# Kernel optimization log

Measured on AMD Instinct MI355X. Metric: run time of the kernel, lower is better.

## Reference

```python
import jax, jax.numpy as jnp
import numpy as np

DEPTH = 16
HID = 256
INP = 256
K = 2  # arity of the complete binary tree
TOTAL = (1 << (DEPTH + 1)) - 1  # 131071 nodes, level-order indexed


def setup_inputs() -> dict:
    key = jax.random.key(0)
    ks = jax.random.split(key, 14)
    s = 1.0 / np.sqrt(HID)
    inp = {
        "x": jax.random.normal(ks[0], (TOTAL, INP), jnp.float32),
        "Wi": jax.random.normal(ks[1], (HID, INP), jnp.float32) * s,
        "bi": jax.random.normal(ks[2], (HID,), jnp.float32) * s,
        "Wf": jax.random.normal(ks[3], (HID, INP), jnp.float32) * s,
        "bf": jax.random.normal(ks[4], (HID,), jnp.float32) * s,
        "Wo": jax.random.normal(ks[5], (HID, INP), jnp.float32) * s,
        "bo": jax.random.normal(ks[6], (HID,), jnp.float32) * s,
        "Wu": jax.random.normal(ks[7], (HID, INP), jnp.float32) * s,
        "bu": jax.random.normal(ks[8], (HID,), jnp.float32) * s,
        "Ui": jax.random.normal(ks[9], (HID, HID), jnp.float32) * s,
        "Uo": jax.random.normal(ks[10], (HID, HID), jnp.float32) * s,
        "Uu": jax.random.normal(ks[11], (HID, HID), jnp.float32) * s,
        "Wfk": jax.random.normal(ks[12], (K, HID, HID), jnp.float32) * s,
        "depth": DEPTH,
    }
    return inp


def reference(x, Wi, bi, Wf, bf, Wo, bo, Wu, bu, Ui, Uo, Uu, Wfk, depth):
    sig = jax.nn.sigmoid
    H = Ui.shape[0]
    # leaf level: leaf_forward (no recurrent terms)
    start, n = (1 << depth) - 1, 1 << depth
    xs = x[start:start + n]                      # [n, INP]
    i = sig(xs @ Wi.T + bi)
    o = sig(xs @ Wo.T + bo)
    u = jnp.tanh(xs @ Wu.T + bu)
    c = i * u
    h = o * jnp.tanh(c)
    # internal levels, bottom-up
    for d in range(depth - 1, -1, -1):
        start, n = (1 << d) - 1, 1 << d
        xs = x[start:start + n]                  # [n, INP]
        hc = h.reshape(n, K, H)                  # children h (level-order)
        cc = c.reshape(n, K, H)                  # children c
        Hs = hc.sum(axis=1)                      # sum over children, [n, H]
        i = sig(xs @ Wi.T + bi + Hs @ Ui.T)
        o = sig(xs @ Wo.T + bo + Hs @ Uo.T)
        u = jnp.tanh(xs @ Wu.T + bu + Hs @ Uu.T)
        # per-child-position forget gate; original applies wf{k} to the SUM of all children h
        fx = xs @ Wf.T + bf                      # [n, H]
        ukfh = jnp.einsum('ni,koi->nko', Hs, Wfk)  # [n, K, H]
        f = sig(fx[:, None, :] + ukfh)
        c = i * u + (f * cc).sum(axis=1)
        h = o * jnp.tanh(c)
    return jnp.stack([h, c])  # [2, 1, H]: root (h, c)
```

## Files before the change

kernel.cpp:

```cpp
#include <hip/hip_runtime.h>
#include <math.h>


#define LEAF_N 65536

typedef __attribute__((ext_vector_type(8))) short bf16x8;
typedef __attribute__((ext_vector_type(4))) float f32x4;
typedef __attribute__((ext_vector_type(8))) float f32x8;
typedef __attribute__((ext_vector_type(8))) _Float16 f16x8;
typedef unsigned short u16;

__device__ __forceinline__ float fast_sig(float x) {
    return __builtin_amdgcn_rcpf(1.0f + __expf(-x));
}
__device__ __forceinline__ float fast_tanh(float x) {
    return 2.0f * __builtin_amdgcn_rcpf(1.0f + __expf(-2.0f * x)) - 1.0f;
}

__device__ __forceinline__ u16 f2bf(float f) {
    union { float f; unsigned u; } v; v.f = f;
    unsigned r = v.u + 0x7fffu + ((v.u >> 16) & 1u);
    return (u16)(r >> 16);
}

__host__ __device__ __forceinline__ size_t zrowOff(int d) {
    return (size_t)(65536 - (2 << d)) * 512;
}

__device__ __forceinline__ void gld_lds16(const u16* g, u16* s) {
    __builtin_amdgcn_global_load_lds(
        (const __attribute__((address_space(1))) void*)g,
        (__attribute__((address_space(3))) void*)s, 16, 0, 0);
}

__global__ __launch_bounds__(256) void pack_weights(
    const float* __restrict__ Wi, const float* __restrict__ bi,
    const float* __restrict__ Wf, const float* __restrict__ bf,
    const float* __restrict__ Wo, const float* __restrict__ bo,
    const float* __restrict__ Wu, const float* __restrict__ bu,
    const float* __restrict__ Ui, const float* __restrict__ Uo,
    const float* __restrict__ Uu, const float* __restrict__ Wfk,
    u16* __restrict__ Wrow, u16* __restrict__ Wfrag, u16* __restrict__ WleafRow,
    float* __restrict__ bbig, float* __restrict__ bleaf)
{
    int idx = blockIdx.x * 256 + threadIdx.x;
    const int NWB = 1280 * 512;
    const int NWL = 768 * 256;

    auto bigval = [&](int row, int k) -> float {
        int g = row >> 8, rr = row & 255;
        if (k < 256) {
            const float* W = (g == 0) ? Wi : (g == 1) ? Wo : (g == 2) ? Wu : Wf;
            return W[rr * 256 + k];
        }
        int kk = k - 256;
        return (g == 0) ? Ui[rr * 256 + kk]
             : (g == 1) ? Uo[rr * 256 + kk]
             : (g == 2) ? Uu[rr * 256 + kk]
             : (g == 3) ? Wfk[rr * 256 + kk]
                        : Wfk[65536 + rr * 256 + kk];
    };

    if (idx < NWB) {
        Wrow[idx] = f2bf(bigval(idx >> 9, idx & 511));
    } else if (idx < 2 * NWB) {
        int q = idx - NWB;
        int j = q & 7, l = (q >> 3) & 63, kc = (q >> 9) & 15, nt = q >> 13;
        int row = nt * 16 + (l & 15);
        int k = kc * 32 + ((l >> 4) << 3) + j;
        Wfrag[q] = f2bf(bigval(row, k));
    } else if (idx < 2 * NWB + NWL) {
        int q = idx - 2 * NWB;
        int r = q >> 8, k = q & 255;
        int g = r >> 8, rr = r & 255;
        const float* W = (g == 0) ? Wi : (g == 1) ? Wo : Wu;
        WleafRow[q] = f2bf(W[rr * 256 + k]);
    } else if (idx < 2 * NWB + NWL + 1280) {
        int r = idx - 2 * NWB - NWL;
        int g = r >> 8, rr = r & 255;
        bbig[r] = (g == 0) ? bi[rr] : (g == 1) ? bo[rr] : (g == 2) ? bu[rr] : bf[rr];
    } else if (idx < 2 * NWB + NWL + 1280 + 768) {
        int r = idx - 2 * NWB - NWL - 1280;
        int g = r >> 8, rr = r & 255;
        bleaf[r] = (g == 0) ? bi[rr] : (g == 1) ? bo[rr] : bu[rr];
    }
}

__global__ __launch_bounds__(256) void cvt_all(
    const float* __restrict__ x, u16* __restrict__ Zrow,
    u16* __restrict__ Ztiles, u16* __restrict__ Xbf)
{
    int idx = blockIdx.x * 256 + threadIdx.x;
    if (idx >= 131071 * 32) return;
    int row = idx >> 5, k8 = idx & 31;
    const float* s = x + (size_t)row * 256 + k8 * 8;
    u16 r[8];
#pragma unroll
    for (int i = 0; i < 8; i++) r[i] = f2bf(s[i]);
    if (row < 65535) {
        int d = 31 - __clz(row + 1);
        int jn = row - ((1 << d) - 1);
        if (d >= 5) {
            *(uint4*)(Zrow + zrowOff(d) + (size_t)jn * 512 + k8 * 8) = *(uint4*)r;
        } else {
            int kc = k8 >> 2;
            int l = (jn & 15) + ((k8 & 3) << 4);
            size_t dst = (size_t)(4 - d) * 8192 + ((size_t)kc * 64 + l) * 8;
            *(uint4*)(Ztiles + dst) = *(uint4*)r;
        }
    } else {
        int jn = row - 65535;
        *(uint4*)(Xbf + (size_t)jn * 256 + k8 * 8) = *(uint4*)r;
    }
}

template<int KD, int NC>
__global__ __launch_bounds__(512, 2) void gate_gemm_big(
    const u16* __restrict__ A, const u16* __restrict__ B,
    const float* __restrict__ bias, _Float16* __restrict__ G)
{
    constexpr int NT = KD / 64;
    extern __shared__ u16 S[];

    const int tid  = threadIdx.x;
    const int wave = tid >> 6;
    const int lane = tid & 63;
    const int bm = blockIdx.x * 256;
    const int bn = blockIdx.y * 256;

    const int srow = lane >> 3;
    const int scol = ((lane & 7) ^ srow) * 8;

    const int wr = wave >> 2;
    const int wc = wave & 3;
    const int lm = lane & 15, q4 = lane >> 4;

    auto stage = [&](int bi, int t) {
#pragma unroll
        for (int q = 0; q < 4; ++q) {
            const int g = wave * 4 + q;
            const int r = g * 8 + srow;
            gld_lds16(A + (size_t)(bm + r) * KD + t * 64 + scol,
                      S + bi * 32768 + g * 512 + lane * 8);
            gld_lds16(B + (size_t)(bn + r) * KD + t * 64 + scol,
                      S + bi * 32768 + 16384 + g * 512 + lane * 8);
        }
    };

    f32x4 acc[8][4] = {};

    stage(0, 0);
    __syncthreads();

#pragma unroll
    for (int t = 0; t < NT; ++t) {
        if (t + 1 < NT) stage((t + 1) & 1, t + 1);

        const u16* Ab = S + (t & 1) * 32768;
        const u16* Bb = Ab + 16384;
#pragma unroll
        for (int kk = 0; kk < 64; kk += 32) {
            const int sw = ((((kk >> 3) + q4) ^ (lm & 7)) << 3);
            bf16x8 af[8], bfr[4];
#pragma unroll
            for (int i = 0; i < 8; i++)
                af[i] = *(const bf16x8*)(Ab + (wr * 128 + i * 16 + lm) * 64 + sw);
#pragma unroll
            for (int j = 0; j < 4; j++)
                bfr[j] = *(const bf16x8*)(Bb + (wc * 64 + j * 16 + lm) * 64 + sw);
#pragma unroll
            for (int i = 0; i < 8; i++)
#pragma unroll
                for (int j = 0; j < 4; j++)
                    acc[i][j] = __builtin_amdgcn_mfma_f32_16x16x32_bf16(
                        af[i], bfr[j], acc[i][j], 0, 0, 0);
        }
        __syncthreads();
    }

    const int cr0 = q4 * 4;
#pragma unroll
    for (int i = 0; i < 8; i++) {
#pragma unroll
        for (int j = 0; j < 4; j++) {
            const int cg = bn + wc * 64 + j * 16 + lm;
            const float bb = bias[cg];
            const bool istan = ((cg >> 8) == 2);
#pragma unroll
            for (int reg = 0; reg < 4; reg++) {
                const int rr = bm + wr * 128 + i * 16 + cr0 + reg;
                float v = acc[i][j][reg] + bb;
                G[(size_t)rr * NC + cg] =
                    (_Float16)(istan ? fast_tanh(v) : fast_sig(v));
            }
        }
    }
}

__global__ __launch_bounds__(256) void gate_gemm(
    const u16* __restrict__ A, int lda, int M,
    const u16* __restrict__ B, int ldb, int Kdim,
    const float* __restrict__ bias, _Float16* __restrict__ G, int NC)
{
    __shared__ u16 As[128 * 64];
    __shared__ u16 Bs[128 * 64];

    const int tid  = threadIdx.x;
    const int wave = tid >> 6;
    const int lane = tid & 63;
    const int bm = blockIdx.x * 128;
    const int bn = blockIdx.y * 128;

    const int wm = (wave >> 1) * 64;
    const int wn = (wave & 1) * 64;
    const int lm = lane & 15;
    const int q4 = lane >> 4;

    const int srow = lane >> 3;
    const int scol = ((lane & 7) ^ srow) * 8;

    f32x4 acc[4][4] = {};

    for (int k0 = 0; k0 < Kdim; k0 += 64) {
#pragma unroll
        for (int q = 0; q < 4; ++q) {
            const int grp = wave * 4 + q;
            const int r = grp * 8 + srow;
            gld_lds16(A + (size_t)(bm + r) * lda + k0 + scol,
                      As + (size_t)grp * 512 + lane * 8);
            gld_lds16(B + (size_t)(bn + r) * ldb + k0 + scol,
                      Bs + (size_t)grp * 512 + lane * 8);
        }
        __syncthreads();

#pragma unroll
        for (int kk = 0; kk < 64; kk += 32) {
            const int sw = (((kk >> 3) + q4) ^ (lm & 7)) << 3;
            bf16x8 af[4], bfr[4];
#pragma unroll
            for (int i = 0; i < 4; i++)
                af[i] = *(const bf16x8*)(As + (wm + i * 16 + lm) * 64 + sw);
#pragma unroll
            for (int j = 0; j < 4; j++)
                bfr[j] = *(const bf16x8*)(Bs + (wn + j * 16 + lm) * 64 + sw);
#pragma unroll
            for (int i = 0; i < 4; i++)
#pragma unroll
                for (int j = 0; j < 4; j++)
                    acc[i][j] = __builtin_amdgcn_mfma_f32_16x16x32_bf16(
                        af[i], bfr[j], acc[i][j], 0, 0, 0);
        }
        __syncthreads();
    }

    const int cr0 = q4 * 4;
    const int ccc = lm;
#pragma unroll
    for (int i = 0; i < 4; i++) {
#pragma unroll
        for (int reg = 0; reg < 4; reg++) {
            int r = bm + wm + i * 16 + cr0 + reg;
            if (r >= M) continue;
#pragma unroll
            for (int j = 0; j < 4; j++) {
                int cn = bn + wn + j * 16 + ccc;
                float v = acc[i][j][reg] + bias[cn];
                float a = ((cn >> 8) == 2) ? fast_tanh(v) : fast_sig(v);
                G[(size_t)r * NC + cn] = (_Float16)a;
            }
        }
    }
}

template<bool LEAF>
__global__ __launch_bounds__(256) void combine_v(
    const _Float16* __restrict__ G, const float* __restrict__ csrc,
    float* __restrict__ cdst, u16* __restrict__ zrow_parent,
    u16* __restrict__ zfrag_parent)
{
    constexpr int NC = LEAF ? 768 : 1280;
    const int t  = threadIdx.x;
    const int p  = blockIdx.x * 8 + (t >> 5);
    const int h0 = (t & 31) * 8;

    const _Float16* G0 = G + (size_t)(2 * p) * NC + h0;
    const _Float16* G1 = G0 + NC;

    f16x8 i0 = *(const f16x8*)(G0);
    f16x8 o0 = *(const f16x8*)(G0 + 256);
    f16x8 u0 = *(const f16x8*)(G0 + 512);
    f16x8 i1 = *(const f16x8*)(G1);
    f16x8 o1 = *(const f16x8*)(G1 + 256);
    f16x8 u1 = *(const f16x8*)(G1 + 512);

    f32x8 c0, c1;
#pragma unroll
    for (int e = 0; e < 8; e++) {
        c0[e] = (float)i0[e] * (float)u0[e];
        c1[e] = (float)i1[e] * (float)u1[e];
    }
    if (!LEAF) {
        f16x8 f00 = *(const f16x8*)(G0 + 768);
        f16x8 f10 = *(const f16x8*)(G0 + 1024);
        f16x8 f01 = *(const f16x8*)(G1 + 768);
        f16x8 f11 = *(const f16x8*)(G1 + 1024);
        const float* cs = csrc + (size_t)(4 * p) * 256 + h0;
        f32x8 cc0 = *(const f32x8*)(cs);
        f32x8 cc1 = *(const f32x8*)(cs + 256);
        f32x8 cc2 = *(const f32x8*)(cs + 512);
        f32x8 cc3 = *(const f32x8*)(cs + 768);
#pragma unroll
        for (int e = 0; e < 8; e++) {
            c0[e] += (float)f00[e] * cc0[e] + (float)f10[e] * cc1[e];
            c1[e] += (float)f01[e] * cc2[e] + (float)f11[e] * cc3[e];
        }
    }

    u16 hs[8];
#pragma unroll
    for (int e = 0; e < 8; e++) {
        float h0v = (float)o0[e] * fast_tanh(c0[e]);
        float h1v = (float)o1[e] * fast_tanh(c1[e]);
        hs[e] = f2bf(h0v + h1v);
    }

    float* cd = cdst + (size_t)(2 * p) * 256 + h0;
    *(f32x8*)(cd) = c0;
    *(f32x8*)(cd + 256) = c1;

    if (zrow_parent) {
        *(uint4*)(zrow_parent + (size_t)p * 512 + 256 + h0) = *(uint4*)hs;
    } else {
        size_t a = (((size_t)8 + (h0 >> 5)) * 64
                    + (p & 15) + (((h0 >> 3) & 3) << 4)) * 8;
        *(uint4*)(zfrag_parent + a) = *(uint4*)hs;
    }
}

__global__ __launch_bounds__(64) void small_gemm(
    const u16* __restrict__ Zpk, const u16* __restrict__ Wfrag,
    const float* __restrict__ bias, float* __restrict__ pre, int n)
{
    const int lane = threadIdx.x;
    const int q = blockIdx.x;
    const int nt0 = (q >> 2) * 16 + (q & 3) * 4;
    const int cc = lane & 15, rq = (lane >> 4) * 4;

    f32x4 acc[4] = {};
    const u16* aB = Zpk + (size_t)lane * 8;
    const u16* bB = Wfrag + ((size_t)nt0 * 16 * 64 + lane) * 8;

    bf16x8 aX, bX[4], aY, bY[4];
    aX = *(const bf16x8*)(aB);
#pragma unroll
    for (int j = 0; j < 4; ++j)
        bX[j] = *(const bf16x8*)(bB + (size_t)(j * 16) * 512);

#pragma unroll
    for (int kc = 0; kc < 16; kc += 2) {
        aY = *(const bf16x8*)(aB + (size_t)(kc + 1) * 512);
#pragma unroll
        for (int j = 0; j < 4; ++j)
            bY[j] = *(const bf16x8*)(bB + (size_t)(j * 16 + kc + 1) * 512);
#pragma unroll
        for (int j = 0; j < 4; ++j)
            acc[j] = __builtin_amdgcn_mfma_f32_16x16x32_bf16(aX, bX[j], acc[j], 0, 0, 0);
        if (kc + 2 < 16) {
            aX = *(const bf16x8*)(aB + (size_t)(kc + 2) * 512);
#pragma unroll
            for (int j = 0; j < 4; ++j)
                bX[j] = *(const bf16x8*)(bB + (size_t)(j * 16 + kc + 2) * 512);
        }
#pragma unroll
        for (int j = 0; j < 4; ++j)
            acc[j] = __builtin_amdgcn_mfma_f32_16x16x32_bf16(aY, bY[j], acc[j], 0, 0, 0);
    }

#pragma unroll
    for (int j = 0; j < 4; ++j) {
        int coln = (nt0 + j) * 16 + cc;
        float bb = bias[coln];
#pragma unroll
        for (int r = 0; r < 4; ++r) {
            int row = rq + r;
            if (row < n) pre[(size_t)row * 1280 + coln] = acc[j][r] + bb;
        }
    }
}

__global__ __launch_bounds__(256) void epi_small(
    const float* __restrict__ pre, const float* __restrict__ csrc,
    float* __restrict__ c_out, u16* __restrict__ zfrag_parent,
    float* __restrict__ root_out, int npairs)
{
    int idx = blockIdx.x * 256 + threadIdx.x;
    if (root_out) {
        int h = idx;
        const float* p = pre;
        float c = fast_sig(p[h]) * fast_tanh(p[512 + h])
                + fast_sig(p[768 + h]) * csrc[h]
                + fast_sig(p[1024 + h]) * csrc[256 + h];
        root_out[h] = fast_sig(p[256 + h]) * fast_tanh(c);
        root_out[256 + h] = c;
        return;
    }
    if (idx >= npairs * 256) return;
    int pI = idx >> 8, h = idx & 255;
    int n0 = 2 * pI;
    const float* p0 = pre + (size_t)n0 * 1280;
    const float* p1 = p0 + 1280;
    float c0 = fast_sig(p0[h]) * fast_tanh(p0[512 + h])
             + fast_sig(p0[768 + h]) * csrc[(size_t)(2 * n0) * 256 + h]
             + fast_sig(p0[1024 + h]) * csrc[(size_t)(2 * n0 + 1) * 256 + h];
    float c1 = fast_sig(p1[h]) * fast_tanh(p1[512 + h])
             + fast_sig(p1[768 + h]) * csrc[(size_t)(2 * n0 + 2) * 256 + h]
             + fast_sig(p1[1024 + h]) * csrc[(size_t)(2 * n0 + 3) * 256 + h];
    float h0 = fast_sig(p0[256 + h]) * fast_tanh(c0);
    float h1 = fast_sig(p1[256 + h]) * fast_tanh(c1);
    c_out[(size_t)n0 * 256 + h] = c0;
    c_out[(size_t)(n0 + 1) * 256 + h] = c1;
    size_t a = (((size_t)8 + (h >> 5)) * 64
                + (pI & 15) + (((h >> 3) & 3) << 4)) * 8 + (h & 7);
    zfrag_parent[a] = f2bf(h0 + h1);
}

extern "C" void kernel_launch(void* const* d_in, const int* in_sizes, int n_in,
                              void* d_out, int out_size, void* d_ws, size_t ws_size,
                              hipStream_t stream)
{
    const float* x   = (const float*)d_in[0];
    const float* Wi  = (const float*)d_in[1];
    const float* bi  = (const float*)d_in[2];
    const float* Wf  = (const float*)d_in[3];
    const float* bf  = (const float*)d_in[4];
    const float* Wo  = (const float*)d_in[5];
    const float* bo  = (const float*)d_in[6];
    const float* Wu  = (const float*)d_in[7];
    const float* bu  = (const float*)d_in[8];
    const float* Ui  = (const float*)d_in[9];
    const float* Uo  = (const float*)d_in[10];
    const float* Uu  = (const float*)d_in[11];
    const float* Wfk = (const float*)d_in[12];
    float* out = (float*)d_out;
    char* ws   = (char*)d_ws;
    (void)ws_size; (void)in_sizes; (void)n_in; (void)out_size;

    size_t off = 0;
    u16* Wrow     = (u16*)(ws + off); off += (size_t)1280 * 512 * 2;
    u16* Wfrag    = (u16*)(ws + off); off += (size_t)1280 * 512 * 2;
    u16* WleafRow = (u16*)(ws + off); off += (size_t)768 * 256 * 2;
    float* bbig   = (float*)(ws + off); off += 1280 * 4;
    float* bleaf  = (float*)(ws + off); off += 768 * 4 + 192;
    u16* Xbf    = (u16*)(ws + off); off += (size_t)65536 * 256 * 2;
    u16* Zrow   = (u16*)(ws + off); off += (size_t)65536 * 512 * 2;
    u16* Ztiles = (u16*)(ws + off); off += (size_t)5 * 8192 * 2;
    float* cA = (float*)(ws + off); off += (size_t)65536 * 256 * 4;
    float* cB = (float*)(ws + off); off += (size_t)32768 * 256 * 4;
    float* pre_small = (float*)(ws + off); off += (size_t)16 * 1280 * 4;
    _Float16* Ghalf = (_Float16*)(ws + off); off += (size_t)65536 * 768 * 2;

    auto ztile = [&](int d) -> u16* { return Ztiles + (size_t)(4 - d) * 8192; };

    static bool attr_set = false;
    if (!attr_set) {
        hipFuncSetAttribute((const void*)gate_gemm_big<512, 1280>,
                            hipFuncAttributeMaxDynamicSharedMemorySize, 131072);
        hipFuncSetAttribute((const void*)gate_gemm_big<256, 768>,
                            hipFuncAttributeMaxDynamicSharedMemorySize, 131072);
        attr_set = true;
    }

    pack_weights<<<5897, 256, 0, stream>>>(Wi, bi, Wf, bf, Wo, bo, Wu, bu,
                                           Ui, Uo, Uu, Wfk, Wrow, Wfrag, WleafRow,
                                           bbig, bleaf);
    cvt_all<<<16385, 256, 0, stream>>>(x, Zrow, Ztiles, Xbf);

    gate_gemm_big<256, 768><<<dim3(LEAF_N / 256, 3), 512, 131072, stream>>>(
        Xbf, WleafRow, bleaf, Ghalf);
    combine_v<true><<<LEAF_N / 16, 256, 0, stream>>>(
        Ghalf, nullptr, cA, Zrow + zrowOff(15), nullptr);

    for (int d = 15; d >= 5; d--) {
        int n = 1 << d;
        float* csrc = (d & 1) ? cA : cB;
        float* cdst = (d & 1) ? cB : cA;
        if (d >= 13) {
            gate_gemm_big<512, 1280><<<dim3(n / 256, 5), 512, 131072, stream>>>(
                Zrow + zrowOff(d), Wrow, bbig, Ghalf);
        } else {
            gate_gemm<<<dim3((n + 127) / 128, 10), 256, 0, stream>>>(
                Zrow + zrowOff(d), 512, n, Wrow, 512, 512, bbig, Ghalf, 1280);
        }
        if (d >= 6)
            combine_v<false><<<n / 16, 256, 0, stream>>>(
                Ghalf, csrc, cdst, Zrow + zrowOff(d - 1), nullptr);
        else
            combine_v<false><<<n / 16, 256, 0, stream>>>(
                Ghalf, csrc, cdst, nullptr, ztile(4));
    }

    for (int d = 4; d >= 1; d--) {
        int n = 1 << d;
        float* csrc = (d & 1) ? cA : cB;
        float* cdst = (d & 1) ? cB : cA;
        small_gemm<<<20, 64, 0, stream>>>(ztile(d), Wfrag, bbig, pre_small, n);
        epi_small<<<n / 2, 256, 0, stream>>>(pre_small, csrc, cdst,
                                             ztile(d - 1), nullptr, n / 2);
    }

    small_gemm<<<20, 64, 0, stream>>>(ztile(0), Wfrag, bbig, pre_small, 1);
    epi_small<<<1, 256, 0, stream>>>(pre_small, cB, nullptr, nullptr, out, 0);
}
```

Before: 794.0 us.

## Fuse gate GEMM and cell update into one kernel for levels 11 to root

Measured after the change: 1.123 ms. +41.4%, slower.

```diff
diff --git a/kernel.cpp b/kernel.cpp
--- a/kernel.cpp
+++ b/kernel.cpp
@@ -88,7 +88,7 @@
 
 __global__ __launch_bounds__(256) void cvt_all(
     const float* __restrict__ x, u16* __restrict__ Zrow,
-    u16* __restrict__ Ztiles, u16* __restrict__ Xbf)
+    u16* __restrict__ Xbf)
 {
     int idx = blockIdx.x * 256 + threadIdx.x;
     if (idx >= 131071 * 32) return;
@@ -100,14 +100,7 @@
     if (row < 65535) {
         int d = 31 - __clz(row + 1);
         int jn = row - ((1 << d) - 1);
-        if (d >= 5) {
-            *(uint4*)(Zrow + zrowOff(d) + (size_t)jn * 512 + k8 * 8) = *(uint4*)r;
-        } else {
-            int kc = k8 >> 2;
-            int l = (jn & 15) + ((k8 & 3) << 4);
-            size_t dst = (size_t)(4 - d) * 8192 + ((size_t)kc * 64 + l) * 8;
-            *(uint4*)(Ztiles + dst) = *(uint4*)r;
-        }
+        *(uint4*)(Zrow + zrowOff(d) + (size_t)jn * 512 + k8 * 8) = *(uint4*)r;
     } else {
         int jn = row - 65535;
         *(uint4*)(Xbf + (size_t)jn * 256 + k8 * 8) = *(uint4*)r;
@@ -275,8 +268,7 @@
 template<bool LEAF>
 __global__ __launch_bounds__(256) void combine_v(
     const _Float16* __restrict__ G, const float* __restrict__ csrc,
-    float* __restrict__ cdst, u16* __restrict__ zrow_parent,
-    u16* __restrict__ zfrag_parent)
+    float* __restrict__ cdst, u16* __restrict__ zrow_parent)
 {
     constexpr int NC = LEAF ? 768 : 1280;
     const int t  = threadIdx.x;
@@ -328,100 +320,82 @@
     *(f32x8*)(cd) = c0;
     *(f32x8*)(cd + 256) = c1;
 
-    if (zrow_parent) {
-        *(uint4*)(zrow_parent + (size_t)p * 512 + 256 + h0) = *(uint4*)hs;
-    } else {
-        size_t a = (((size_t)8 + (h0 >> 5)) * 64
-                    + (p & 15) + (((h0 >> 3) & 3) << 4)) * 8;
-        *(uint4*)(zfrag_parent + a) = *(uint4*)hs;
-    }
-}
-
-__global__ __launch_bounds__(64) void small_gemm(
-    const u16* __restrict__ Zpk, const u16* __restrict__ Wfrag,
-    const float* __restrict__ bias, float* __restrict__ pre, int n)
-{
-    const int lane = threadIdx.x;
-    const int q = blockIdx.x;
-    const int nt0 = (q >> 2) * 16 + (q & 3) * 4;
+    *(uint4*)(zrow_parent + (size_t)p * 512 + 256 + h0) = *(uint4*)hs;
+}
+
+__global__ __launch_bounds__(256) void fused_level(
+    const u16* __restrict__ Z, const u16* __restrict__ Wfrag,
+    const float* __restrict__ bbig, const float* __restrict__ csrc,
+    float* __restrict__ cdst, u16* __restrict__ zp,
+    float* __restrict__ out, int n)
+{
+    const int lane = threadIdx.x & 63;
+    const int w = threadIdx.x >> 6;
+    const int r0 = blockIdx.x * 16;
     const int cc = lane & 15, rq = (lane >> 4) * 4;
 
-    f32x4 acc[4] = {};
-    const u16* aB = Zpk + (size_t)lane * 8;
-    const u16* bB = Wfrag + ((size_t)nt0 * 16 * 64 + lane) * 8;
-
-    bf16x8 aX, bX[4], aY, bY[4];
-    aX = *(const bf16x8*)(aB);
-#pragma unroll
-    for (int j = 0; j < 4; ++j)
-        bX[j] = *(const bf16x8*)(bB + (size_t)(j * 16) * 512);
-
-#pragma unroll
-    for (int kc = 0; kc < 16; kc += 2) {
-        aY = *(const bf16x8*)(aB + (size_t)(kc + 1) * 512);
-#pragma unroll
-        for (int j = 0; j < 4; ++j)
-            bY[j] = *(const bf16x8*)(bB + (size_t)(j * 16 + kc + 1) * 512);
-#pragma unroll
-        for (int j = 0; j < 4; ++j)
-            acc[j] = __builtin_amdgcn_mfma_f32_16x16x32_bf16(aX, bX[j], acc[j], 0, 0, 0);
-        if (kc + 2 < 16) {
-            aX = *(const bf16x8*)(aB + (size_t)(kc + 2) * 512);
-#pragma unroll
-            for (int j = 0; j < 4; ++j)
-                bX[j] = *(const bf16x8*)(bB + (size_t)(j * 16 + kc + 2) * 512);
-        }
-#pragma unroll
-        for (int j = 0; j < 4; ++j)
-            acc[j] = __builtin_amdgcn_mfma_f32_16x16x32_bf16(aY, bY[j], acc[j], 0, 0, 0);
-    }
-
-#pragma unroll
-    for (int j = 0; j < 4; ++j) {
-        int coln = (nt0 + j) * 16 + cc;
-        float bb = bias[coln];
+    f32x4 acc[5][4] = {};
+
+    const int arow = min(r0 + cc, n - 1);
+    const u16* aB = Z + (size_t)arow * 512 + (lane >> 4) * 8;
+
+#pragma unroll 2
+    for (int kc = 0; kc < 16; ++kc) {
+        bf16x8 av = *(const bf16x8*)(aB + kc * 32);
+#pragma unroll
+        for (int g = 0; g < 5; ++g)
+#pragma unroll
+            for (int jt = 0; jt < 4; ++jt) {
+                const int nt = g * 16 + w * 4 + jt;
+                bf16x8 bv = *(const bf16x8*)(Wfrag +
+                    ((size_t)(nt * 16 + kc) * 64 + lane) * 8);
+                acc[g][jt] = __builtin_amdgcn_mfma_f32_16x16x32_bf16(
+                    av, bv, acc[g][jt], 0, 0, 0);
+            }
+    }
+
+#pragma unroll
+    for (int jt = 0; jt < 4; ++jt) {
+        const int h = (w * 4 + jt) * 16 + cc;
+        const float bI = bbig[h],        bO = bbig[256 + h];
+        const float bU = bbig[512 + h],  bF0 = bbig[768 + h];
+        const float bF1 = bbig[1024 + h];
+        float cr[4], hr[4];
 #pragma unroll
         for (int r = 0; r < 4; ++r) {
-            int row = rq + r;
-            if (row < n) pre[(size_t)row * 1280 + coln] = acc[j][r] + bb;
-        }
-    }
-}
-
-__global__ __launch_bounds__(256) void epi_small(
-    const float* __restrict__ pre, const float* __restrict__ csrc,
-    float* __restrict__ c_out, u16* __restrict__ zfrag_parent,
-    float* __restrict__ root_out, int npairs)
-{
-    int idx = blockIdx.x * 256 + threadIdx.x;
-    if (root_out) {
-        int h = idx;
-        const float* p = pre;
-        float c = fast_sig(p[h]) * fast_tanh(p[512 + h])
-                + fast_sig(p[768 + h]) * csrc[h]
-                + fast_sig(p[1024 + h]) * csrc[256 + h];
-        root_out[h] = fast_sig(p[256 + h]) * fast_tanh(c);
-        root_out[256 + h] = c;
-        return;
-    }
-    if (idx >= npairs * 256) return;
-    int pI = idx >> 8, h = idx & 255;
-    int n0 = 2 * pI;
-    const float* p0 = pre + (size_t)n0 * 1280;
-    const float* p1 = p0 + 1280;
-    float c0 = fast_sig(p0[h]) * fast_tanh(p0[512 + h])
-             + fast_sig(p0[768 + h]) * csrc[(size_t)(2 * n0) * 256 + h]
-             + fast_sig(p0[1024 + h]) * csrc[(size_t)(2 * n0 + 1) * 256 + h];
-    float c1 = fast_sig(p1[h]) * fast_tanh(p1[512 + h])
-             + fast_sig(p1[768 + h]) * csrc[(size_t)(2 * n0 + 2) * 256 + h]
-             + fast_sig(p1[1024 + h]) * csrc[(size_t)(2 * n0 + 3) * 256 + h];
-    float h0 = fast_sig(p0[256 + h]) * fast_tanh(c0);
-    float h1 = fast_sig(p1[256 + h]) * fast_tanh(c1);
-    c_out[(size_t)n0 * 256 + h] = c0;
-    c_out[(size_t)(n0 + 1) * 256 + h] = c1;
-    size_t a = (((size_t)8 + (h >> 5)) * 64
-                + (pI & 15) + (((h >> 3) & 3) << 4)) * 8 + (h & 7);
-    zfrag_parent[a] = f2bf(h0 + h1);
+            const int row = r0 + rq + r;
+            float cv = 0.f, hv = 0.f;
+            if (row < n) {
+                float i  = fast_sig(acc[0][jt][r] + bI);
+                float o  = fast_sig(acc[1][jt][r] + bO);
+                float u  = fast_tanh(acc[2][jt][r] + bU);
+                float f0 = fast_sig(acc[3][jt][r] + bF0);
+                float f1 = fast_sig(acc[4][jt][r] + bF1);
+                cv = i * u
+                   + f0 * csrc[(size_t)(2 * row) * 256 + h]
+                   + f1 * csrc[(size_t)(2 * row + 1) * 256 + h];
+                hv = o * fast_tanh(cv);
+            }
+            cr[r] = cv; hr[r] = hv;
+        }
+        if (out) {
+            if (rq == 0) { out[h] = hr[0]; out[256 + h] = cr[0]; }
+        } else {
+#pragma unroll
+            for (int r = 0; r < 4; ++r) {
+                const int row = r0 + rq + r;
+                if (row < n) cdst[(size_t)row * 256 + h] = cr[r];
+            }
+#pragma unroll
+            for (int s = 0; s < 2; ++s) {
+                const int row = r0 + rq + 2 * s;
+                if (row < n) {
+                    const int pp = row >> 1;
+                    zp[(size_t)pp * 512 + 256 + h] = f2bf(hr[2 * s] + hr[2 * s + 1]);
+                }
+            }
+        }
+    }
 }
 
 extern "C" void kernel_launch(void* const* d_in, const int* in_sizes, int n_in,
@@ -453,13 +427,9 @@
     float* bleaf  = (float*)(ws + off); off += 768 * 4 + 192;
     u16* Xbf    = (u16*)(ws + off); off += (size_t)65536 * 256 * 2;
     u16* Zrow   = (u16*)(ws + off); off += (size_t)65536 * 512 * 2;
-    u16* Ztiles = (u16*)(ws + off); off += (size_t)5 * 8192 * 2;
     float* cA = (float*)(ws + off); off += (size_t)65536 * 256 * 4;
     float* cB = (float*)(ws + off); off += (size_t)32768 * 256 * 4;
-    float* pre_small = (float*)(ws + off); off += (size_t)16 * 1280 * 4;
     _Float16* Ghalf = (_Float16*)(ws + off); off += (size_t)65536 * 768 * 2;
-
-    auto ztile = [&](int d) -> u16* { return Ztiles + (size_t)(4 - d) * 8192; };
 
     static bool attr_set = false;
     if (!attr_set) {
@@ -473,14 +443,14 @@
     pack_weights<<<5897, 256, 0, stream>>>(Wi, bi, Wf, bf, Wo, bo, Wu, bu,
                                            Ui, Uo, Uu, Wfk, Wrow, Wfrag, WleafRow,
                                            bbig, bleaf);
-    cvt_all<<<16385, 256, 0, stream>>>(x, Zrow, Ztiles, Xbf);
+    cvt_all<<<16385, 256, 0, stream>>>(x, Zrow, Xbf);
 
     gate_gemm_big<256, 768><<<dim3(LEAF_N / 256, 3), 512, 131072, stream>>>(
         Xbf, WleafRow, bleaf, Ghalf);
     combine_v<true><<<LEAF_N / 16, 256, 0, stream>>>(
-        Ghalf, nullptr, cA, Zrow + zrowOff(15), nullptr);
-
-    for (int d = 15; d >= 5; d--) {
+        Ghalf, nullptr, cA, Zrow + zrowOff(15));
+
+    for (int d = 15; d >= 12; d--) {
         int n = 1 << d;
         float* csrc = (d & 1) ? cA : cB;
         float* cdst = (d & 1) ? cB : cA;
@@ -488,26 +458,23 @@
             gate_gemm_big<512, 1280><<<dim3(n / 256, 5), 512, 131072, stream>>>(
                 Zrow + zrowOff(d), Wrow, bbig, Ghalf);
         } else {
-            gate_gemm<<<dim3((n + 127) / 128, 10), 256, 0, stream>>>(
+            gate_gemm<<<dim3(n / 128, 10), 256, 0, stream>>>(
                 Zrow + zrowOff(d), 512, n, Wrow, 512, 512, bbig, Ghalf, 1280);
         }
-        if (d >= 6)
-            combine_v<false><<<n / 16, 256, 0, stream>>>(
-                Ghalf, csrc, cdst, Zrow + zrowOff(d - 1), nullptr);
-        else
-            combine_v<false><<<n / 16, 256, 0, stream>>>(
-                Ghalf, csrc, cdst, nullptr, ztile(4));
-    }
-
-    for (int d = 4; d >= 1; d--) {
+        combine_v<false><<<n / 16, 256, 0, stream>>>(
+            Ghalf, csrc, cdst, Zrow + zrowOff(d - 1));
+    }
+
+    for (int d = 11; d >= 1; d--) {
         int n = 1 << d;
         float* csrc = (d & 1) ? cA : cB;
         float* cdst = (d & 1) ? cB : cA;
-        small_gemm<<<20, 64, 0, stream>>>(ztile(d), Wfrag, bbig, pre_small, n);
-        epi_small<<<n / 2, 256, 0, stream>>>(pre_small, csrc, cdst,
-                                             ztile(d - 1), nullptr, n / 2);
-    }
-
-    small_gemm<<<20, 64, 0, stream>>>(ztile(0), Wfrag, bbig, pre_small, 1);
-    epi_small<<<1, 256, 0, stream>>>(pre_small, cB, nullptr, nullptr, out, 0);
-}
+        int blocks = (n + 15) / 16;
+        fused_level<<<blocks, 256, 0, stream>>>(
+            Zrow + zrowOff(d), Wfrag, bbig, csrc, cdst,
+            Zrow + zrowOff(d - 1), nullptr, n);
+    }
+
+    fused_level<<<1, 256, 0, stream>>>(
+        Zrow + zrowOff(0), Wfrag, bbig, cB, nullptr, nullptr, out, 1);
+}
```
